# Kernel tuning notes

Hardware: AMD Instinct MI355X
Metric: run time of the kernel (lower is better)

The kernel has to match this reference:

```python
import jax, jax.numpy as jnp
import numpy as np

B = 8          # events per batch
NPB = 8192     # points per event (equal counts -> Nmax = NPB)
N = B * NPB
FEAT = 6
K = 128        # max_tokens
TOK = 768      # token_dim
KNN = 16       # k_neighbors
MLP_DIMS = [FEAT, 256, 512, 768, TOK]


def setup_inputs() -> dict:
    key = jax.random.key(0)
    ks = jax.random.split(key, 20)
    coords = jax.random.normal(ks[0], (N, 3), jnp.float32) * 5.0
    features = jax.random.normal(ks[1], (N, FEAT), jnp.float32)
    times = jax.random.uniform(ks[2], (N, 1), jnp.float32)
    # equal-sized, sorted batch ids (8192 points per event)
    batch_ids = jnp.repeat(jnp.arange(B, dtype=jnp.int32), NPB)
    inp = {"coords": coords, "features": features, "batch_ids": batch_ids, "times": times}
    # per-point MLP: 6 -> 256 -> 512 -> 768 -> 768 (last Linear has no ReLU)
    ki = 3
    for i in range(4):
        din, dout = MLP_DIMS[i], MLP_DIMS[i + 1]
        inp[f"W{i+1}"] = jax.random.normal(ks[ki], (din, dout), jnp.float32) / np.sqrt(din); ki += 1
        inp[f"b{i+1}"] = jnp.zeros((dout,), jnp.float32)
    # neighborhood MLP: 768 -> 768 -> 768
    inp["Wn1"] = jax.random.normal(ks[ki], (TOK, TOK), jnp.float32) / np.sqrt(TOK); ki += 1
    inp["bn1"] = jnp.zeros((TOK,), jnp.float32)
    inp["Wn2"] = jax.random.normal(ks[ki], (TOK, TOK), jnp.float32) / np.sqrt(TOK); ki += 1
    inp["bn2"] = jnp.zeros((TOK,), jnp.float32)
    return inp


def _forward(coords, features, batch_ids, times,
             W1, b1, W2, b2, W3, b3, W4, b4, Wn1, bn1, Wn2, bn2):
    INF = jnp.float32(jnp.inf)
    points4 = jnp.concatenate([coords[:, :3], times], axis=-1)  # [N,4] (x,y,z,t)
    # per-point MLP
    h = jax.nn.relu(features @ W1 + b1)
    h = jax.nn.relu(h @ W2 + b2)
    h = jax.nn.relu(h @ W3 + b3)
    feats = h @ W4 + b4                                          # [N,TOK]
    # ---- pack flat -> padded [B, NPB, *] ----
    counts = jnp.bincount(batch_ids, length=B)                   # [B]
    offsets = jnp.cumsum(counts) - counts
    pos = jnp.arange(N) - offsets[batch_ids]
    P = jnp.zeros((B, NPB, 4), points4.dtype).at[batch_ids, pos].set(points4)
    Fp = jnp.zeros((B, NPB, TOK), feats.dtype).at[batch_ids, pos].set(feats)
    valid = jnp.arange(NPB)[None, :] < counts[:, None]           # [B,NPB]
    # ---- small path: take first K points sorted by time ----
    tsort = jnp.where(valid, P[..., 3], INF)
    sorted_idx = jnp.argsort(tsort, axis=1)[:, :K]               # K <= NPB
    tokens_small = jnp.take_along_axis(Fp, sorted_idx[..., None], axis=1)
    cents_small = jnp.take_along_axis(P, sorted_idx[..., None], axis=1)
    masks_small = jnp.arange(K)[None, :] < jnp.minimum(counts, K)[:, None]
    tokens_small = tokens_small * masks_small[..., None]
    cents_small = cents_small * masks_small[..., None]
    # ---- batched FPS over 4D points ----
    min_d0 = jnp.where(valid, INF, 0.0)
    norms = jnp.where(valid, jnp.sum(P * P, axis=-1), -INF)
    first = jnp.argmax(norms, axis=1)                            # farthest-from-origin start
    barange = jnp.arange(B)
    def fps_step(carry, _):
        min_d, last = carry
        c = P[barange, last]                                     # [B,4]
        d = jnp.sum((P - c[:, None, :]) ** 2, axis=-1)
        d = jnp.where(valid, d, INF)
        min_d = jnp.minimum(min_d, d)
        return (min_d, jnp.argmax(min_d, axis=1)), last
    _, idx_seq = jax.lax.scan(fps_step, (min_d0, first), None, length=K)
    fps_idx = idx_seq.T                                          # [B,K]
    validK = jnp.arange(K)[None, :] < jnp.minimum(counts, K)[:, None]
    cents_large = jnp.take_along_axis(P, fps_idx[..., None], axis=1)  # [B,K,4]
    # ---- kNN pooling around centroids ----
    diff = cents_large[:, :, None, :] - P[:, None, :, :]         # [B,K,NPB,4]
    dists = jnp.sum(diff * diff, axis=-1)                        # [B,K,NPB]
    dists = jnp.where(valid[:, None, :], dists, INF)
    k_g = min(KNN, NPB)
    _, knn_idx = jax.lax.top_k(-dists, k_g)                      # smallest-k -> [B,K,k]
    knn_valid = jnp.take_along_axis(jnp.broadcast_to(valid[:, None, :], (B, K, NPB)), knn_idx, axis=2)
    neigh = jnp.take_along_axis(Fp[:, None, :, :], knn_idx[..., None], axis=2)  # [B,K,k,TOK]
    masked = jnp.where(knn_valid[..., None], neigh, -INF)
    pooled = jnp.max(masked, axis=2)
    pooled = jnp.where(jnp.isfinite(pooled), pooled, 0.0)
    tokens_large = jax.nn.relu(pooled @ Wn1 + bn1) @ Wn2 + bn2   # [B,K,TOK]
    # sort selected tokens by centroid time
    ctimes = jnp.where(validK, cents_large[..., 3], INF)
    order = jnp.argsort(ctimes, axis=1)
    tokens_large = jnp.take_along_axis(tokens_large, order[..., None], axis=1)
    cents_large = jnp.take_along_axis(cents_large, order[..., None], axis=1)
    masks_large = jnp.take_along_axis(validK, order, axis=1)
    tokens_large = tokens_large * masks_large[..., None]
    cents_large = cents_large * masks_large[..., None]
    # ---- select per-event path ----
    small = counts <= K
    tokens = jnp.where(small[:, None, None], tokens_small, tokens_large)
    cents = jnp.where(small[:, None, None], cents_small, cents_large)
    masks = jnp.where(small[:, None], masks_small, masks_large)
    return tokens, cents, masks


def reference(coords, features, batch_ids, times,
              W1, b1, W2, b2, W3, b3, W4, b4, Wn1, bn1, Wn2, bn2):
    return _forward(coords, features, batch_ids, times,
                    W1, b1, W2, b2, W3, b3, W4, b4, Wn1, bn1, Wn2, bn2)
```

## Files before the change

### kernel.cpp

```cpp
#include <hip/hip_runtime.h>
#include <hip/hip_bf16.h>


#define BEV 8
#define NPB 8192
#define FEAT 6
#define KTOK 128
#define TOK 768
#define KNN 16

typedef unsigned short ushort_t;
typedef unsigned long long u64;
typedef __bf16 bf16x8 __attribute__((ext_vector_type(8)));
typedef float f32x4 __attribute__((ext_vector_type(4)));
typedef float f32x2 __attribute__((ext_vector_type(2)));

__device__ __forceinline__ ushort_t f2b(float f) {
    union { float f; unsigned int i; } x; x.f = f;
    unsigned int i = x.i;
    unsigned int r = (i + 0x7FFFu + ((i >> 16) & 1u)) >> 16;
    return (ushort_t)r;
}

#define DPP_ROW_SHR1  0x111
#define DPP_ROW_SHR2  0x112
#define DPP_ROW_SHR4  0x114
#define DPP_ROW_SHR8  0x118
#define DPP_ROW_BC15  0x142
#define DPP_ROW_BC31  0x143

template <int CTRL>
__device__ __forceinline__ float dpp_fmax(float v) {
    int o = __builtin_amdgcn_update_dpp(__float_as_int(v), __float_as_int(v),
                                        CTRL, 0xf, 0xf, false);
    return fmaxf(v, __int_as_float(o));
}

template <int CTRL>
__device__ __forceinline__ u64 dpp_u64max(u64 k) {
    int lo = (int)(unsigned)(k & 0xFFFFFFFFu);
    int hi = (int)(unsigned)(k >> 32);
    unsigned olo = (unsigned)__builtin_amdgcn_update_dpp(lo, lo, CTRL, 0xf, 0xf, false);
    unsigned ohi = (unsigned)__builtin_amdgcn_update_dpp(hi, hi, CTRL, 0xf, 0xf, false);
    u64 o = ((u64)ohi << 32) | (u64)olo;
    return o > k ? o : k;
}

__global__ __launch_bounds__(256) void fill_kernel(float* __restrict__ out, int n) {
    int i = blockIdx.x * 256 + threadIdx.x;
    if (i < n) out[i] = 0.f;
}

__global__ __launch_bounds__(1024) void fps_kernel(
    const float* __restrict__ coords, const float* __restrict__ times,
    float* __restrict__ cents, int* __restrict__ pos,
    float* __restrict__ cents_out, float* __restrict__ masks_out)
{
#pragma clang fp contract(off)
    const int b = blockIdx.x;
    const int t = threadIdx.x;
    __shared__ u64   slotk[2][16];
    __shared__ float tarr[KTOK];
    __shared__ float carr[KTOK][4];
    f32x2 px[4], py[4], pz[4], pw[4], md[4];
    const long base = (long)b * NPB;
#pragma unroll
    for (int i = 0; i < 4; ++i) {
        long g = base + t * 8 + i * 2;
        px[i] = (f32x2){coords[g * 3 + 0], coords[(g + 1) * 3 + 0]};
        py[i] = (f32x2){coords[g * 3 + 1], coords[(g + 1) * 3 + 1]};
        pz[i] = (f32x2){coords[g * 3 + 2], coords[(g + 1) * 3 + 2]};
        pw[i] = (f32x2){times[g], times[g + 1]};
        md[i] = (f32x2){__builtin_inff(), __builtin_inff()};
    }
    const int wv = t >> 6, lane = t & 63;
    float cx = 0.f, cy = 0.f, cz = 0.f, cw = 0.f;
    for (int s = 0; s < KTOK; ++s) {
        f32x2 v[4];
        if (s == 0) {
#pragma unroll
            for (int i = 0; i < 4; ++i)
                v[i] = ((px[i]*px[i] + py[i]*py[i]) + pz[i]*pz[i]) + pw[i]*pw[i];
        } else {
            const f32x2 c2x = {cx, cx}, c2y = {cy, cy}, c2z = {cz, cz}, c2w = {cw, cw};
#pragma unroll
            for (int i = 0; i < 4; ++i) {
                f32x2 dx = px[i] - c2x, dy = py[i] - c2y;
                f32x2 dz = pz[i] - c2z, dw = pw[i] - c2w;
                f32x2 d = ((dx*dx + dy*dy) + dz*dz) + dw*dw;
                md[i] = __builtin_elementwise_min(md[i], d);
                v[i] = md[i];
            }
        }
        f32x2 m01 = __builtin_elementwise_max(v[0], v[1]);
        f32x2 m23 = __builtin_elementwise_max(v[2], v[3]);
        f32x2 mm  = __builtin_elementwise_max(m01, m23);
        const float bv = fmaxf(mm[0], mm[1]);
        float mvv = bv;
        mvv = dpp_fmax<DPP_ROW_SHR1>(mvv);
        mvv = dpp_fmax<DPP_ROW_SHR2>(mvv);
        mvv = dpp_fmax<DPP_ROW_SHR4>(mvv);
        mvv = dpp_fmax<DPP_ROW_SHR8>(mvv);
        mvv = dpp_fmax<DPP_ROW_BC15>(mvv);
        mvv = dpp_fmax<DPP_ROW_BC31>(mvv);
        const float mv = __int_as_float(__builtin_amdgcn_readlane(__float_as_int(mvv), 63));
        const u64 mask = __ballot(bv == mv);
        const int wl = __ffsll((long long)mask) - 1;
        const int p = s & 1;
        if (lane == wl) {
            int bi = t * 8;
#pragma unroll
            for (int j = 7; j >= 0; --j)
                if (v[j >> 1][j & 1] == mv) bi = t * 8 + j;
            slotk[p][wv] = ((u64)__float_as_uint(mv) << 32)
                         | (unsigned)(NPB - 1 - bi);
        }
        __syncthreads();
        u64 k1 = slotk[p][lane & 15];
        k1 = dpp_u64max<DPP_ROW_SHR1>(k1);
        k1 = dpp_u64max<DPP_ROW_SHR2>(k1);
        k1 = dpp_u64max<DPP_ROW_SHR4>(k1);
        k1 = dpp_u64max<DPP_ROW_SHR8>(k1);
        const unsigned klo =
            (unsigned)__builtin_amdgcn_readlane((int)(unsigned)(k1 & 0xFFFFFFFFu), 15);
        const int widx = NPB - 1 - (int)klo;
        const long gc = base + widx;
        cx = coords[gc * 3 + 0]; cy = coords[gc * 3 + 1];
        cz = coords[gc * 3 + 2]; cw = times[gc];
        if (t == 0) {
            tarr[s] = cw;
            carr[s][0] = cx; carr[s][1] = cy; carr[s][2] = cz; carr[s][3] = cw;
        }
    }
    __syncthreads();
    if (t < KTOK) {
        const float ti = tarr[t];
        int rank = 0;
        for (int j = 0; j < KTOK; ++j) {
            float tj = tarr[j];
            if (tj < ti || (tj == ti && j < t)) ++rank;
        }
        rank &= (KTOK - 1);
        pos[b * KTOK + t] = rank;
        float* cc = &cents[(b * KTOK + t) * 4];
        cc[0] = carr[t][0]; cc[1] = carr[t][1];
        cc[2] = carr[t][2]; cc[3] = carr[t][3];
#pragma unroll
        for (int c = 0; c < 4; ++c)
            cents_out[(b * KTOK + rank) * 4 + c] = carr[t][c];
        masks_out[b * KTOK + t] = 1.0f;
    }
}

__global__ __launch_bounds__(256) void knn_tc(
    const float* __restrict__ coords, const float* __restrict__ times,
    const float* __restrict__ cents, int* __restrict__ knn_idx,
    const float* __restrict__ W2, ushort_t* __restrict__ Wt2,
    const float* __restrict__ W3, ushort_t* __restrict__ Wt3,
    const float* __restrict__ W4, ushort_t* __restrict__ Wt4)
{
#pragma clang fp contract(off)
    __shared__ float tile[32][33];
    __shared__ float rv[4];
    __shared__ int   ri[4];
    const int blk = blockIdx.x;
    if (blk >= BEV * KTOK) {
        const int id = blk - BEV * KTOK;
        const float* in; ushort_t* out; int K, N, bx, by;
        if (id < 128)      { in = W2; out = Wt2; K = 256; N = 512;
                             bx = id & 15; by = id >> 4; }
        else if (id < 512) { in = W3; out = Wt3; K = 512; N = 768;
                             int r = id - 128; bx = r % 24; by = r / 24; }
        else               { in = W4; out = Wt4; K = 768; N = 768;
                             int r = id - 512; bx = r % 24; by = r / 24; }
        const int tt = threadIdx.x, tx = tt & 31, ty = tt >> 5;
#pragma unroll
        for (int r = 0; r < 4; ++r) {
            int y = by * 32 + ty + r * 8;
            tile[ty + r * 8][tx] = in[(long)y * N + bx * 32 + tx];
        }
        __syncthreads();
        const int ko = by * 32 + tx;
#pragma unroll
        for (int r = 0; r < 4; ++r) {
            int no = bx * 32 + ty + r * 8;
            out[(long)no * K + ko] = f2b(tile[tx][ty + r * 8]);
        }
        return;
    }
    const int b = blk >> 7;
    const int t = threadIdx.x;
    const float cx = cents[blk*4+0], cy = cents[blk*4+1];
    const float cz = cents[blk*4+2], cw = cents[blk*4+3];
    float d[32];
    const long base = (long)b * NPB;
#pragma unroll
    for (int i = 0; i < 32; ++i) {
        long g = base + t * 32 + i;
        float dx = coords[g*3+0] - cx;
        float dy = coords[g*3+1] - cy;
        float dz = coords[g*3+2] - cz;
        float dw = times[g] - cw;
        d[i] = ((dx*dx + dy*dy) + dz*dz) + dw*dw;
    }
    const int wv = t >> 6, lane = t & 63;
    for (int pass = 0; pass < KNN; ++pass) {
        float bvv = __builtin_inff(); int bii = t * 32;
#pragma unroll
        for (int i = 0; i < 32; ++i)
            if (d[i] < bvv) { bvv = d[i]; bii = t * 32 + i; }
        for (int off = 1; off < 64; off <<= 1) {
            float ov = __shfl_xor(bvv, off);
            int   oi = __shfl_xor(bii, off);
            if (ov < bvv || (ov == bvv && oi < bii)) { bvv = ov; bii = oi; }
        }
        if (lane == 0) { rv[wv] = bvv; ri[wv] = bii; }
        __syncthreads();
        float gb = __builtin_inff(); int winner = 0;
        for (int wI = 0; wI < 4; ++wI) {
            float v = rv[wI]; int idx = ri[wI];
            if (v < gb || (v == gb && idx < winner)) { gb = v; winner = idx; }
        }
        winner &= (NPB - 1);
#pragma unroll
        for (int i = 0; i < 32; ++i)
            if (t * 32 + i == winner) d[i] = __builtin_inff();
        if (t == 0) knn_idx[blk * KNN + pass] = winner;
        __syncthreads();
    }
}

#define PAD1 264
#define PAD2 520
#define PAD3 776
__global__ __launch_bounds__(512) void mlp_fused(
    const float* __restrict__ features, const float* __restrict__ W1,
    const float* __restrict__ b1, const int* __restrict__ knn_idx,
    const ushort_t* __restrict__ Wt2, const float* __restrict__ b2,
    const ushort_t* __restrict__ Wt3, const float* __restrict__ b3,
    const ushort_t* __restrict__ Wt4, const float* __restrict__ b4,
    ushort_t* __restrict__ pooled)
{
    __shared__ __align__(16) ushort_t lds[67712];
    ushort_t* h1 = lds;
    ushort_t* h2 = lds + 16896;
    ushort_t* h3 = lds;
    ushort_t* Bs = lds + 50176;
    float*    feat = (float*)(lds + 66560);
    int*      pidx = (int*)(lds + 67584);

    const int bi = blockIdx.x;
    const int t = threadIdx.x;
    const int w = t >> 6, lane = t & 63;
    const int ln = lane & 15, q = lane >> 4;
    const int mg = w >> 2;
    const int wn = w & 3;

    if (t < 64) {
        const int c = bi * 4 + (t >> 4);
        const int ev = c >> 7;
        pidx[t] = ev * NPB + (knn_idx[c * KNN + (t & 15)] & (NPB - 1));
    }
    __syncthreads();
    if (t < 384) {
        const int r = t / 6, f = t - r * 6;
        feat[r * 8 + f] = features[(long)pidx[r] * FEAT + f];
    }
    __syncthreads();
    {
        const int col = t & 255, half = t >> 8;
        float wv[FEAT];
#pragma unroll
        for (int f = 0; f < FEAT; ++f) wv[f] = W1[f * 256 + col];
        const float bias = b1[col];
#pragma unroll
        for (int r = 0; r < 32; ++r) {
            const int row = half * 32 + r;
            float acc = 0.f;
#pragma unroll
            for (int f = 0; f < FEAT; ++f) acc += feat[row * 8 + f] * wv[f];
            h1[row * PAD1 + col] = f2b(fmaxf(acc + bias, 0.f));
        }
    }
    __syncthreads();

    {
        f32x4 acc[2][8];
#pragma unroll
        for (int m = 0; m < 2; ++m)
#pragma unroll
            for (int i = 0; i < 8; ++i) acc[m][i] = (f32x4){0,0,0,0};
        for (int k0 = 0; k0 < 256; k0 += 64) {
            bf16x8 af[2][2];
#pragma unroll
            for (int m = 0; m < 2; ++m)
#pragma unroll
                for (int kh = 0; kh < 2; ++kh)
                    af[m][kh] = *(const bf16x8*)(&h1[(mg * 32 + m * 16 + ln) * PAD1 + k0 + kh * 32 + q * 8]);
#pragma unroll
            for (int np = 0; np < 2; ++np) {
                __syncthreads();
#pragma unroll
                for (int i = 0; i < 4; ++i) {
                    int e = t + i * 512, n = e >> 3, sk = e & 7;
                    *(uint4*)(&Bs[n * 64 + ((sk ^ (n & 7)) * 8)]) =
                        *(const uint4*)(Wt2 + (long)(np * 256 + n) * 256 + k0 + sk * 8);
                }
                __syncthreads();
#pragma unroll
                for (int j = 0; j < 4; ++j) {
                    const int row = (wn * 4 + j) * 16 + ln;
                    bf16x8 bf0 = *(const bf16x8*)(&Bs[row * 64 + ((q ^ (row & 7)) * 8)]);
                    bf16x8 bf1 = *(const bf16x8*)(&Bs[row * 64 + (((4 + q) ^ (row & 7)) * 8)]);
#pragma unroll
                    for (int m = 0; m < 2; ++m) {
                        acc[m][np * 4 + j] = __builtin_amdgcn_mfma_f32_16x16x32_bf16(af[m][0], bf0, acc[m][np * 4 + j], 0, 0, 0);
                        acc[m][np * 4 + j] = __builtin_amdgcn_mfma_f32_16x16x32_bf16(af[m][1], bf1, acc[m][np * 4 + j], 0, 0, 0);
                    }
                }
            }
        }
        __syncthreads();
#pragma unroll
        for (int np = 0; np < 2; ++np)
#pragma unroll
            for (int j = 0; j < 4; ++j) {
                const int col = np * 256 + (wn * 4 + j) * 16 + ln;
                const float bias = b2[col];
#pragma unroll
                for (int m = 0; m < 2; ++m)
#pragma unroll
                    for (int r = 0; r < 4; ++r)
                        h2[(mg * 32 + m * 16 + q * 4 + r) * PAD2 + col] = f2b(fmaxf(acc[m][np * 4 + j][r] + bias, 0.f));
            }
    }
    __syncthreads();

    {
        f32x4 acc[2][12];
#pragma unroll
        for (int m = 0; m < 2; ++m)
#pragma unroll
            for (int i = 0; i < 12; ++i) acc[m][i] = (f32x4){0,0,0,0};
        for (int k0 = 0; k0 < 512; k0 += 64) {
            bf16x8 af[2][2];
#pragma unroll
            for (int m = 0; m < 2; ++m)
#pragma unroll
                for (int kh = 0; kh < 2; ++kh)
                    af[m][kh] = *(const bf16x8*)(&h2[(mg * 32 + m * 16 + ln) * PAD2 + k0 + kh * 32 + q * 8]);
#pragma unroll
            for (int np = 0; np < 3; ++np) {
                __syncthreads();
#pragma unroll
                for (int i = 0; i < 4; ++i) {
                    int e = t + i * 512, n = e >> 3, sk = e & 7;
                    *(uint4*)(&Bs[n * 64 + ((sk ^ (n & 7)) * 8)]) =
                        *(const uint4*)(Wt3 + (long)(np * 256 + n) * 512 + k0 + sk * 8);
                }
                __syncthreads();
#pragma unroll
                for (int j = 0; j < 4; ++j) {
                    const int row = (wn * 4 + j) * 16 + ln;
                    bf16x8 bf0 = *(const bf16x8*)(&Bs[row * 64 + ((q ^ (row & 7)) * 8)]);
                    bf16x8 bf1 = *(const bf16x8*)(&Bs[row * 64 + (((4 + q) ^ (row & 7)) * 8)]);
#pragma unroll
                    for (int m = 0; m < 2; ++m) {
                        acc[m][np * 4 + j] = __builtin_amdgcn_mfma_f32_16x16x32_bf16(af[m][0], bf0, acc[m][np * 4 + j], 0, 0, 0);
                        acc[m][np * 4 + j] = __builtin_amdgcn_mfma_f32_16x16x32_bf16(af[m][1], bf1, acc[m][np * 4 + j], 0, 0, 0);
                    }
                }
            }
        }
        __syncthreads();
#pragma unroll
        for (int np = 0; np < 3; ++np)
#pragma unroll
            for (int j = 0; j < 4; ++j) {
                const int col = np * 256 + (wn * 4 + j) * 16 + ln;
                const float bias = b3[col];
#pragma unroll
                for (int m = 0; m < 2; ++m)
#pragma unroll
                    for (int r = 0; r < 4; ++r)
                        h3[(mg * 32 + m * 16 + q * 4 + r) * PAD3 + col] = f2b(fmaxf(acc[m][np * 4 + j][r] + bias, 0.f));
            }
    }
    __syncthreads();

    {
        f32x4 acc[2][12];
#pragma unroll
        for (int m = 0; m < 2; ++m)
#pragma unroll
            for (int i = 0; i < 12; ++i) acc[m][i] = (f32x4){0,0,0,0};
        for (int k0 = 0; k0 < 768; k0 += 64) {
            bf16x8 af[2][2];
#pragma unroll
            for (int m = 0; m < 2; ++m)
#pragma unroll
                for (int kh = 0; kh < 2; ++kh)
                    af[m][kh] = *(const bf16x8*)(&h3[(mg * 32 + m * 16 + ln) * PAD3 + k0 + kh * 32 + q * 8]);
#pragma unroll
            for (int np = 0; np < 3; ++np) {
                __syncthreads();
#pragma unroll
                for (int i = 0; i < 4; ++i) {
                    int e = t + i * 512, n = e >> 3, sk = e & 7;
                    *(uint4*)(&Bs[n * 64 + ((sk ^ (n & 7)) * 8)]) =
                        *(const uint4*)(Wt4 + (long)(np * 256 + n) * 768 + k0 + sk * 8);
                }
                __syncthreads();
#pragma unroll
                for (int j = 0; j < 4; ++j) {
                    const int row = (wn * 4 + j) * 16 + ln;
                    bf16x8 bf0 = *(const bf16x8*)(&Bs[row * 64 + ((q ^ (row & 7)) * 8)]);
                    bf16x8 bf1 = *(const bf16x8*)(&Bs[row * 64 + (((4 + q) ^ (row & 7)) * 8)]);
#pragma unroll
                    for (int m = 0; m < 2; ++m) {
                        acc[m][np * 4 + j] = __builtin_amdgcn_mfma_f32_16x16x32_bf16(af[m][0], bf0, acc[m][np * 4 + j], 0, 0, 0);
                        acc[m][np * 4 + j] = __builtin_amdgcn_mfma_f32_16x16x32_bf16(af[m][1], bf1, acc[m][np * 4 + j], 0, 0, 0);
                    }
                }
            }
        }
#pragma unroll
        for (int np = 0; np < 3; ++np)
#pragma unroll
            for (int j = 0; j < 4; ++j) {
                const int col = np * 256 + (wn * 4 + j) * 16 + ln;
#pragma unroll
                for (int m = 0; m < 2; ++m) {
                    float v = fmaxf(fmaxf(acc[m][np * 4 + j][0], acc[m][np * 4 + j][1]),
                                    fmaxf(acc[m][np * 4 + j][2], acc[m][np * 4 + j][3]));
                    v = fmaxf(v, __shfl_xor(v, 16));
                    v = fmaxf(v, __shfl_xor(v, 32));
                    if (q == 0)
                        pooled[(long)(bi * 4 + mg * 2 + m) * TOK + col] = f2b(v + b4[col]);
                }
            }
    }
}

template<int EPI, int RELU, int F32OUT>
__global__ __launch_bounds__(256) void gemm64_kn(
    const ushort_t* __restrict__ A, const float* __restrict__ B,
    const float* __restrict__ bias, void* __restrict__ Cv,
    int M, int N, int Kd, const int* __restrict__ pos)
{
    __shared__ __align__(16) ushort_t As[64 * 40];
    __shared__ __align__(16) ushort_t Bsh[64 * 40];
    ushort_t* Cb = (ushort_t*)Cv;
    float*    Cf = (float*)Cv;
    const int tid = threadIdx.x;
    const int m0 = blockIdx.x * 64;
    const int n0 = blockIdx.y * 64;
    const int w = tid >> 6, lane = tid & 63;
    const int ln = lane & 15, q = lane >> 4;
    f32x4 acc[4];
#pragma unroll
    for (int ni = 0; ni < 4; ++ni) acc[ni] = (f32x4){0.f, 0.f, 0.f, 0.f};

    const int ar = tid >> 2, as0 = (tid & 3) * 8;
    const int kk = tid >> 4, nn = (tid & 15) * 4;

    for (int k0 = 0; k0 < Kd; k0 += 32) {
        __syncthreads();
        uint4 a0 = *(const uint4*)(A + (long)(m0 + ar) * Kd + k0 + as0);
        float4 f0 = *(const float4*)(B + (long)(k0 + kk)      * N + n0 + nn);
        float4 f1 = *(const float4*)(B + (long)(k0 + kk + 16) * N + n0 + nn);
        *(uint4*)(&As[ar * 40 + as0]) = a0;
        float e0[4] = {f0.x, f0.y, f0.z, f0.w};
        float e1[4] = {f1.x, f1.y, f1.z, f1.w};
#pragma unroll
        for (int j = 0; j < 4; ++j) Bsh[(nn + j) * 40 + kk]      = f2b(e0[j]);
#pragma unroll
        for (int j = 0; j < 4; ++j) Bsh[(nn + j) * 40 + kk + 16] = f2b(e1[j]);
        __syncthreads();
        bf16x8 af = *(const bf16x8*)(&As[(w * 16 + ln) * 40 + q * 8]);
#pragma unroll
        for (int ni = 0; ni < 4; ++ni) {
            bf16x8 bf = *(const bf16x8*)(&Bsh[(ni * 16 + ln) * 40 + q * 8]);
            acc[ni] = __builtin_amdgcn_mfma_f32_16x16x32_bf16(af, bf, acc[ni], 0, 0, 0);
        }
    }

#pragma unroll
    for (int ni = 0; ni < 4; ++ni) {
        const int col = n0 + ni * 16 + ln;
        const float bv = bias[col];
#pragma unroll
        for (int r = 0; r < 4; ++r) {
            const int row = m0 + w * 16 + q * 4 + r;
            float v = acc[ni][r] + bv;
            if (EPI == 0) {
                if (RELU) v = fmaxf(v, 0.f);
                if (F32OUT) Cf[(long)row * N + col] = v;
                else        Cb[(long)row * N + col] = f2b(v);
            } else {
                const int orow = (row & ~(KTOK - 1)) + (pos[row] & (KTOK - 1));
                if (F32OUT) Cf[(long)orow * N + col] = v;
                else        Cb[(long)orow * N + col] = f2b(v);
            }
        }
    }
}

extern "C" void kernel_launch(void* const* d_in, const int* in_sizes, int n_in,
                              void* d_out, int out_size, void* d_ws, size_t ws_size,
                              hipStream_t stream)
{
    const float* coords   = (const float*)d_in[0];
    const float* features = (const float*)d_in[1];
    const float* times    = (const float*)d_in[3];
    const float* W1  = (const float*)d_in[4];
    const float* b1  = (const float*)d_in[5];
    const float* W2  = (const float*)d_in[6];
    const float* b2  = (const float*)d_in[7];
    const float* W3  = (const float*)d_in[8];
    const float* b3  = (const float*)d_in[9];
    const float* W4  = (const float*)d_in[10];
    const float* b4  = (const float*)d_in[11];
    const float* Wn1 = (const float*)d_in[12];
    const float* bn1 = (const float*)d_in[13];
    const float* Wn2 = (const float*)d_in[14];
    const float* bn2 = (const float*)d_in[15];

    char* ws = (char*)d_ws;
    float*    cents   = (float*)(ws + 0);
    int*      pos     = (int*)(ws + 16384);
    int*      knn_idx = (int*)(ws + 20480);
    ushort_t* t1      = (ushort_t*)(ws + 86016);
    ushort_t* pooled  = (ushort_t*)(ws + 1658880);
    ushort_t* Wt2b    = (ushort_t*)(ws + 3231744);
    ushort_t* Wt3b    = (ushort_t*)(ws + 3493888);
    ushort_t* Wt4b    = (ushort_t*)(ws + 4280320);
    const long WS_NEED = 5459968;

    float* tokens_out = (float*)d_out;
    float* cents_out  = tokens_out + 786432;
    float* masks_out  = tokens_out + 790528;

    if ((long)ws_size < WS_NEED) {
        fill_kernel<<<(791552 + 255) / 256, 256, 0, stream>>>(tokens_out, 791552);
        return;
    }

    fps_kernel<<<BEV, 1024, 0, stream>>>(coords, times, cents, pos,
                                         cents_out, masks_out);

    knn_tc<<<BEV * KTOK + 1088, 256, 0, stream>>>(coords, times, cents, knn_idx,
                                                  W2, Wt2b, W3, Wt3b, W4, Wt4b);

    mlp_fused<<<256, 512, 0, stream>>>(features, W1, b1, knn_idx,
                                       Wt2b, b2, Wt3b, b3, Wt4b, b4, pooled);

    gemm64_kn<0,1,0><<<dim3(16, 12), 256, 0, stream>>>(pooled, Wn1, bn1, t1, 1024, 768, 768, nullptr);
    gemm64_kn<2,0,1><<<dim3(16, 12), 256, 0, stream>>>(t1, Wn2, bn2, tokens_out, 1024, 768, 768, pos);
}
```

Before: 412.7 us.

## Overlap weight transposes with FPS and stage FPS points in LDS

The bf16 weight-transpose work moves from the KNN launch into extra blocks of the FPS launch, so it runs on otherwise idle CUs while the 8 serial FPS blocks execute. The FPS kernel also copies its event's points into padded shared memory and reads each selected centroid from LDS instead of global memory on every one of the 128 serial iterations. The cost is a large static shared allocation (about 135 KB) for every block, including the transpose blocks, which limits residency, and 1024-thread transpose blocks that each handle four tiles.

```diff
diff --git a/kernel.cpp b/kernel.cpp
--- a/kernel.cpp
+++ b/kernel.cpp
@@ -8,6 +8,7 @@
 #define KTOK 128
 #define TOK 768
 #define KNN 16
+#define TCB 272
 
 typedef unsigned short ushort_t;
 typedef unsigned long long u64;
@@ -51,17 +52,48 @@
     if (i < n) out[i] = 0.f;
 }
 
-__global__ __launch_bounds__(1024) void fps_kernel(
+__global__ __launch_bounds__(1024) void fps_tc(
     const float* __restrict__ coords, const float* __restrict__ times,
     float* __restrict__ cents, int* __restrict__ pos,
-    float* __restrict__ cents_out, float* __restrict__ masks_out)
+    float* __restrict__ cents_out, float* __restrict__ masks_out,
+    const float* __restrict__ W2, ushort_t* __restrict__ Wt2,
+    const float* __restrict__ W3, ushort_t* __restrict__ Wt3,
+    const float* __restrict__ W4, ushort_t* __restrict__ Wt4)
 {
 #pragma clang fp contract(off)
-    const int b = blockIdx.x;
+    __shared__ __align__(16) char shmem[137984];
+    const int blk = blockIdx.x;
     const int t = threadIdx.x;
-    __shared__ u64   slotk[2][16];
-    __shared__ float tarr[KTOK];
-    __shared__ float carr[KTOK][4];
+    if (blk >= BEV) {
+        const int id = (blk - BEV) * 4 + (t >> 8);
+        float* tile = (float*)shmem + (t >> 8) * 1056;
+        const int tt = t & 255, tx = tt & 31, ty = tt >> 5;
+        const float* in; ushort_t* out; int K, N, bx, by;
+        if (id < 128)      { in = W2; out = Wt2; K = 256; N = 512;
+                             bx = id & 15; by = id >> 4; }
+        else if (id < 512) { in = W3; out = Wt3; K = 512; N = 768;
+                             int r = id - 128; bx = r % 24; by = r / 24; }
+        else               { in = W4; out = Wt4; K = 768; N = 768;
+                             int r = id - 512; bx = r % 24; by = r / 24; }
+#pragma unroll
+        for (int r = 0; r < 4; ++r) {
+            int y = by * 32 + ty + r * 8;
+            tile[(ty + r * 8) * 33 + tx] = in[(long)y * N + bx * 32 + tx];
+        }
+        __syncthreads();
+        const int ko = by * 32 + tx;
+#pragma unroll
+        for (int r = 0; r < 4; ++r) {
+            int no = bx * 32 + ty + r * 8;
+            out[(long)no * K + ko] = f2b(tile[tx * 33 + ty + r * 8]);
+        }
+        return;
+    }
+    float* pts  = (float*)shmem;
+    u64*   slotk = (u64*)(shmem + 135168);
+    float* tarr = (float*)(shmem + 135424);
+    float* carr = (float*)(shmem + 135936);
+    const int b = blk;
     f32x2 px[4], py[4], pz[4], pw[4], md[4];
     const long base = (long)b * NPB;
 #pragma unroll
@@ -73,6 +105,15 @@
         pw[i] = (f32x2){times[g], times[g + 1]};
         md[i] = (f32x2){__builtin_inff(), __builtin_inff()};
     }
+#pragma unroll
+    for (int i = 0; i < 4; ++i)
+#pragma unroll
+        for (int e = 0; e < 2; ++e) {
+            const int idx = t * 8 + i * 2 + e;
+            const int bf = idx * 4 + t;
+            pts[bf + 0] = px[i][e]; pts[bf + 1] = py[i][e];
+            pts[bf + 2] = pz[i][e]; pts[bf + 3] = pw[i][e];
+        }
     const int wv = t >> 6, lane = t & 63;
     float cx = 0.f, cy = 0.f, cz = 0.f, cw = 0.f;
     for (int s = 0; s < KTOK; ++s) {
@@ -112,11 +153,11 @@
 #pragma unroll
             for (int j = 7; j >= 0; --j)
                 if (v[j >> 1][j & 1] == mv) bi = t * 8 + j;
-            slotk[p][wv] = ((u64)__float_as_uint(mv) << 32)
-                         | (unsigned)(NPB - 1 - bi);
-        }
-        __syncthreads();
-        u64 k1 = slotk[p][lane & 15];
+            slotk[p * 16 + wv] = ((u64)__float_as_uint(mv) << 32)
+                               | (unsigned)(NPB - 1 - bi);
+        }
+        __syncthreads();
+        u64 k1 = slotk[p * 16 + (lane & 15)];
         k1 = dpp_u64max<DPP_ROW_SHR1>(k1);
         k1 = dpp_u64max<DPP_ROW_SHR2>(k1);
         k1 = dpp_u64max<DPP_ROW_SHR4>(k1);
@@ -124,12 +165,13 @@
         const unsigned klo =
             (unsigned)__builtin_amdgcn_readlane((int)(unsigned)(k1 & 0xFFFFFFFFu), 15);
         const int widx = NPB - 1 - (int)klo;
-        const long gc = base + widx;
-        cx = coords[gc * 3 + 0]; cy = coords[gc * 3 + 1];
-        cz = coords[gc * 3 + 2]; cw = times[gc];
+        const int bf = widx * 4 + (widx >> 3);
+        cx = pts[bf + 0]; cy = pts[bf + 1];
+        cz = pts[bf + 2]; cw = pts[bf + 3];
         if (t == 0) {
             tarr[s] = cw;
-            carr[s][0] = cx; carr[s][1] = cy; carr[s][2] = cz; carr[s][3] = cw;
+            carr[s * 4 + 0] = cx; carr[s * 4 + 1] = cy;
+            carr[s * 4 + 2] = cz; carr[s * 4 + 3] = cw;
         }
     }
     __syncthreads();
@@ -143,51 +185,21 @@
         rank &= (KTOK - 1);
         pos[b * KTOK + t] = rank;
         float* cc = &cents[(b * KTOK + t) * 4];
-        cc[0] = carr[t][0]; cc[1] = carr[t][1];
-        cc[2] = carr[t][2]; cc[3] = carr[t][3];
+        cc[0] = carr[t * 4 + 0]; cc[1] = carr[t * 4 + 1];
+        cc[2] = carr[t * 4 + 2]; cc[3] = carr[t * 4 + 3];
 #pragma unroll
         for (int c = 0; c < 4; ++c)
-            cents_out[(b * KTOK + rank) * 4 + c] = carr[t][c];
+            cents_out[(b * KTOK + rank) * 4 + c] = carr[t * 4 + c];
         masks_out[b * KTOK + t] = 1.0f;
     }
 }
 
-__global__ __launch_bounds__(256) void knn_tc(
+__global__ __launch_bounds__(256) void knn_kernel(
     const float* __restrict__ coords, const float* __restrict__ times,
-    const float* __restrict__ cents, int* __restrict__ knn_idx,
-    const float* __restrict__ W2, ushort_t* __restrict__ Wt2,
-    const float* __restrict__ W3, ushort_t* __restrict__ Wt3,
-    const float* __restrict__ W4, ushort_t* __restrict__ Wt4)
+    const float* __restrict__ cents, int* __restrict__ knn_idx)
 {
 #pragma clang fp contract(off)
-    __shared__ float tile[32][33];
-    __shared__ float rv[4];
-    __shared__ int   ri[4];
     const int blk = blockIdx.x;
-    if (blk >= BEV * KTOK) {
-        const int id = blk - BEV * KTOK;
-        const float* in; ushort_t* out; int K, N, bx, by;
-        if (id < 128)      { in = W2; out = Wt2; K = 256; N = 512;
-                             bx = id & 15; by = id >> 4; }
-        else if (id < 512) { in = W3; out = Wt3; K = 512; N = 768;
-                             int r = id - 128; bx = r % 24; by = r / 24; }
-        else               { in = W4; out = Wt4; K = 768; N = 768;
-                             int r = id - 512; bx = r % 24; by = r / 24; }
-        const int tt = threadIdx.x, tx = tt & 31, ty = tt >> 5;
-#pragma unroll
-        for (int r = 0; r < 4; ++r) {
-            int y = by * 32 + ty + r * 8;
-            tile[ty + r * 8][tx] = in[(long)y * N + bx * 32 + tx];
-        }
-        __syncthreads();
-        const int ko = by * 32 + tx;
-#pragma unroll
-        for (int r = 0; r < 4; ++r) {
-            int no = bx * 32 + ty + r * 8;
-            out[(long)no * K + ko] = f2b(tile[tx][ty + r * 8]);
-        }
-        return;
-    }
     const int b = blk >> 7;
     const int t = threadIdx.x;
     const float cx = cents[blk*4+0], cy = cents[blk*4+1];
@@ -203,6 +215,8 @@
         float dw = times[g] - cw;
         d[i] = ((dx*dx + dy*dy) + dz*dz) + dw*dw;
     }
+    __shared__ float rv[4];
+    __shared__ int   ri[4];
     const int wv = t >> 6, lane = t & 63;
     for (int pass = 0; pass < KNN; ++pass) {
         float bvv = __builtin_inff(); int bii = t * 32;
@@ -546,11 +560,11 @@
         return;
     }
 
-    fps_kernel<<<BEV, 1024, 0, stream>>>(coords, times, cents, pos,
-                                         cents_out, masks_out);
-
-    knn_tc<<<BEV * KTOK + 1088, 256, 0, stream>>>(coords, times, cents, knn_idx,
-                                                  W2, Wt2b, W3, Wt3b, W4, Wt4b);
+    fps_tc<<<BEV + TCB, 1024, 0, stream>>>(coords, times, cents, pos,
+                                           cents_out, masks_out,
+                                           W2, Wt2b, W3, Wt3b, W4, Wt4b);
+
+    knn_kernel<<<BEV * KTOK, 256, 0, stream>>>(coords, times, cents, knn_idx);
 
     mlp_fused<<<256, 512, 0, stream>>>(features, W1, b1, knn_idx,
                                        Wt2b, b2, Wt3b, b3, Wt4b, b4, pooled);
```

After: 413.2 us. Within noise of the previous version (+0.1%).
